# Kernel tuning notes

Hardware: AMD Instinct MI355X
Metric: run time of the kernel (lower is better)

## Reference

```python
import jax, jax.numpy as jnp
import numpy as np

EPS = 1e-6
T = 8            # max_recursion_depth
STACK = 16       # stack_size
K = 1024         # n_symbols
CC = 0.25        # commitment_cost
ETH_W = 0.005    # ethical_weight
PONDER = 1e-4    # ponder_penalty
B, DIM, V = 1024, 512, 32000


def _clin(Wr, Wi, zr, zi):
    # complex linear: (Wr + i Wi)(zr + i zi), nn.Linear convention x @ W.T
    return zr @ Wr.T - zi @ Wi.T, zi @ Wr.T + zr @ Wi.T


def _cnorm(scale, shift, zr, zi):
    mag = jnp.sqrt(zr * zr + zi * zi) + EPS
    mean = mag.mean(-1, keepdims=True)
    var = mag.var(-1, keepdims=True, ddof=1)  # torch.var unbiased=True
    nm = (mag - mean) / jnp.sqrt(var + EPS) * scale + shift
    ph = jnp.arctan2(zi, zr)
    return nm * jnp.cos(ph), nm * jnp.sin(ph)


def _modrelu(b, zr, zi):
    n = jnp.sqrt(zr * zr + zi * zi) + EPS
    s = jax.nn.relu(n + b) / n
    return zr * s, zi * s


def setup_inputs() -> dict:
    key = jax.random.key(0)
    ks = jax.random.split(key, 24)
    g = lambda k, sh, s=0.02: (jax.random.normal(k, sh, jnp.float32) * s)
    xav = lambda k, sh: jax.random.uniform(k, sh, jnp.float32, -1, 1) * np.sqrt(6.0 / (sh[0] + sh[1]))
    return {
        'input_ids': jax.random.randint(ks[0], (B, 1), 0, V),
        'emb_mag': g(ks[1], (V, DIM), 1.0),
        'emb_phase': g(ks[2], (V, DIM), 1.0),
        'lin_r': xav(ks[3], (DIM, DIM)), 'lin_i': xav(ks[4], (DIM, DIM)),
        'norm_scale': jnp.ones((DIM,), jnp.float32), 'norm_shift': jnp.zeros((DIM,), jnp.float32),
        'mod_bias': jnp.zeros((DIM,), jnp.float32),
        'halt_W': g(ks[5], (1, 2 * DIM)), 'halt_b': jnp.full((1,), -2.0, jnp.float32),
        'ctrl_W': g(ks[6], (3, 2 * DIM)), 'ctrl_b': jnp.zeros((3,), jnp.float32),
        'q_r': xav(ks[7], (DIM, DIM)), 'q_i': xav(ks[8], (DIM, DIM)),
        'k_r': xav(ks[9], (DIM, DIM)), 'k_i': xav(ks[10], (DIM, DIM)),
        'v_r': xav(ks[11], (DIM, DIM)), 'v_i': xav(ks[12], (DIM, DIM)),
        'codebook': jax.random.normal(ks[13], (K, 2 * DIM), jnp.float32),
        'adjacency': jnp.zeros((K, K), jnp.float32),
        'dec_W': g(ks[14], (V, 2 * DIM)), 'dec_b': jnp.zeros((V,), jnp.float32),
    }


def reference(input_ids, emb_mag, emb_phase, lin_r, lin_i, norm_scale, norm_shift, mod_bias,
              halt_W, halt_b, ctrl_W, ctrl_b, q_r, q_i, k_r, k_i, v_r, v_i,
              codebook, adjacency, dec_W, dec_b):
    dim = emb_mag.shape[1]
    b = input_ids.shape[0]
    idx = input_ids[:, 0]
    r, th = emb_mag[idx], emb_phase[idx]
    zr, zi = r * jnp.cos(th), r * jnp.sin(th)  # [B, dim] complex embedding

    mem = jnp.zeros((b, STACK, 2 * dim), zr.dtype)
    ptr = jnp.zeros((b, STACK), zr.dtype).at[:, 0].set(1.0)
    remain = jnp.ones((b, 1), zr.dtype)
    zwr = jnp.zeros_like(zr); zwi = jnp.zeros_like(zi)
    ponder = jnp.float32(0.0); vq_tot = jnp.float32(0.0)
    eth_tot = jnp.float32(0.0); prev = None
    scale = dim ** -0.5

    for step in range(T):
        # AdaptiveRecursiveCell: linear -> norm -> modrelu -> attention
        pr, pi = _clin(lin_r, lin_i, zr, zi)
        pr, pi = _cnorm(norm_scale, norm_shift, pr, pi)
        pr, pi = _modrelu(mod_bias, pr, pi)
        qr, qi = _clin(q_r, q_i, pr, pi)
        kr, ki = _clin(k_r, k_i, pr, pi)
        vr, vi = _clin(v_r, v_i, pr, pi)
        qf = jnp.concatenate([qr, qi], -1)
        kf = jnp.concatenate([kr, ki], -1)
        A = jax.nn.softmax(qf @ kf.T * scale, -1)  # [B, B] cross-batch attention
        pr, pi = A @ vr, A @ vi
        zf = jnp.concatenate([pr, pi], -1)  # [B, 2dim]
        halt = jax.nn.sigmoid(zf @ halt_W.T + halt_b)        # [B, 1]
        ctrl = jax.nn.softmax(zf @ ctrl_W.T + ctrl_b, -1)    # [B, 3]

        # DifferentiableStack
        push, pop, noop = ctrl[:, :1], ctrl[:, 1:2], ctrl[:, 2:3]
        ptr_up = jnp.roll(ptr, 1, axis=1)
        ptr_dn = jnp.roll(ptr, -1, axis=1)
        nptr = push * ptr_up + pop * ptr_dn + noop * ptr
        nptr = nptr / (nptr.sum(1, keepdims=True) + EPS)
        wm = push * ptr_up  # [B, STACK]
        mem = wm[:, :, None] * zf[:, None, :] + mem * (1.0 - wm[:, :, None])
        read = (mem * nptr[:, :, None]).sum(1)  # [B, 2dim]
        ptr = nptr
        cr = pr + read[:, :dim]; ci = pi + read[:, dim:]

        # GraphMemoryVQ (batched path: graph bias branch is a no-op)
        cf = jnp.concatenate([cr, ci], -1)
        d = ((cf * cf).sum(-1, keepdims=True) + (codebook * codebook).sum(-1)
             - 2.0 * cf @ codebook.T)  # [B, K]
        sym = jnp.argmin(d, -1)
        zq = codebook[sym]
        vq_tot = vq_tot + jnp.mean((zq - jax.lax.stop_gradient(cf)) ** 2) \
                 + CC * jnp.mean((jax.lax.stop_gradient(zq) - cf) ** 2)
        zq = cf + jax.lax.stop_gradient(zq - cf)  # straight-through
        sr, si = zq[:, :dim], zq[:, dim:]

        # EthicalConstraint: cross_entropy(adjacency[prev], curr)
        if prev is not None:
            row = adjacency[prev]  # [B, K]
            eth = jnp.mean(jax.nn.logsumexp(row, -1)
                           - jnp.take_along_axis(row, sym[:, None], 1)[:, 0])
            eth_tot = eth_tot + eth
        prev = sym

        # ACT weighting
        w = remain if step == T - 1 else halt * remain
        zwr = zwr + w * sr; zwi = zwi + w * si
        remain = remain * (1.0 - halt)
        ponder = ponder + remain.mean()
        zr, zi = sr, si

    logits = jnp.concatenate([zwr, zwi], -1) @ dec_W.T + dec_b  # [B, V]
    aux_loss = vq_tot + ETH_W * eth_tot + PONDER * ponder
    return logits, aux_loss
```

## Files before the change

kernel.cpp:

```cpp
#include <hip/hip_runtime.h>
#include <math.h>

#define NB 1024
#define ND 512
#define ND2 1024
#define NSTEPS 8
#define NSTACK 16
#define NK 1024
#define NV 32000
#define FEPS 1e-6f
#define ATT_SCALE 0.044194173824159216f

typedef _Float16 f16;
typedef f16 f16x8 __attribute__((ext_vector_type(8)));
typedef f16 f16x4 __attribute__((ext_vector_type(4)));
typedef float f32x4 __attribute__((ext_vector_type(4)));
typedef unsigned long long u64;

__device__ __forceinline__ int swz(int row, int chunk) {
    return row * 32 + ((chunk ^ ((row >> 1) & 3)) * 8);
}

__device__ __forceinline__ void gl16(const f16* g, f16* l) {
    __builtin_amdgcn_global_load_lds(
        (const __attribute__((address_space(1))) void*)g,
        (__attribute__((address_space(3))) void*)l, 16, 0, 0);
}

__device__ __forceinline__ u64 fkey(float v, int idx) {
    unsigned int ub = __float_as_uint(v);
    unsigned int ord = (ub & 0x80000000u) ? ~ub : (ub | 0x80000000u);
    return ((u64)ord << 32) | (unsigned int)idx;
}

__device__ __forceinline__ void amin_lds(u64* a, u64 k) {
    u64 old = *a;
    while (k < old) {
        u64 prev = atomicCAS(a, old, k);
        if (prev == old) break;
        old = prev;
    }
}

__device__ __forceinline__ float blk_sum(float v, float* red) {
    int t = threadIdx.x;
    red[t] = v; __syncthreads();
    for (int s = 128; s > 0; s >>= 1) {
        if (t < s) red[t] += red[t + s];
        __syncthreads();
    }
    float r = red[0]; __syncthreads();
    return r;
}

__device__ __forceinline__ float blk_max(float v, float* red) {
    int t = threadIdx.x;
    red[t] = v; __syncthreads();
    for (int s = 128; s > 0; s >>= 1) {
        if (t < s) red[t] = fmaxf(red[t], red[t + s]);
        __syncthreads();
    }
    float r = red[0]; __syncthreads();
    return r;
}

__device__ __forceinline__ void split_write(float v, f16* oh, f16* ol, size_t idx) {
    f16 h = (f16)v;
    oh[idx] = h;
    ol[idx] = (f16)((v - (float)h) * 1024.f);
}

__device__ __forceinline__ void buildW_elem(const float* Wr, const float* Wi,
                                            f16* oh, f16* ol, int transp, int idx) {
    int n = idx >> 10, k = idx & 1023;
    int r = transp ? k : n, c = transp ? n : k;
    float v;
    if (r < 512) v = (c < 512) ? Wr[r * 512 + c] : -Wi[r * 512 + (c - 512)];
    else { int r2 = r - 512; v = (c < 512) ? Wi[r2 * 512 + c] : Wr[r2 * 512 + (c - 512)]; }
    split_write(v, oh, ol, idx);
}

__global__ __launch_bounds__(256)
void k_setup(const int* __restrict__ ids, const float* __restrict__ mag,
             const float* __restrict__ phs,
             const float* __restrict__ lin_r, const float* __restrict__ lin_i,
             const float* __restrict__ q_r, const float* __restrict__ q_i,
             const float* __restrict__ k_r, const float* __restrict__ k_i,
             const float* __restrict__ v_r, const float* __restrict__ v_i,
             const float* __restrict__ cb, const float* __restrict__ adj,
             const float* __restrict__ dec_W,
             f16* __restrict__ W1_h, f16* __restrict__ W1_l,
             f16* __restrict__ WqT_h, f16* __restrict__ WqT_l,
             f16* __restrict__ WkT_h, f16* __restrict__ WkT_l,
             f16* __restrict__ Bv_h, f16* __restrict__ Bv_l,
             f16* __restrict__ cb_h, f16* __restrict__ cb_l,
             f16* __restrict__ dW_h,
             f16* __restrict__ zh, f16* __restrict__ zl,
             float* __restrict__ cbn, float* __restrict__ lse,
             float* __restrict__ ptrb, float* __restrict__ remainb,
             float* __restrict__ scal, u64* __restrict__ amin2) {
    __shared__ float red[256];
    int bid = blockIdx.x, t = threadIdx.x;
    if (bid < 4096) {
        buildW_elem(lin_r, lin_i, W1_h, W1_l, 0, bid * 256 + t);
    } else if (bid < 8192) {
        buildW_elem(q_r, q_i, WqT_h, WqT_l, 1, (bid - 4096) * 256 + t);
    } else if (bid < 12288) {
        buildW_elem(k_r, k_i, WkT_h, WkT_l, 1, (bid - 8192) * 256 + t);
    } else if (bid < 16384) {
        buildW_elem(v_r, v_i, Bv_h, Bv_l, 0, (bid - 12288) * 256 + t);
    } else if (bid < 20480) {
        int idx = (bid - 16384) * 256 + t;
        split_write(cb[idx], cb_h, cb_l, idx);
    } else if (bid < 22528) {
        size_t i = (size_t)(bid - 20480) * 256 + t;
        size_t st = (size_t)2048 * 256;
        size_t n = (size_t)NV * ND2;
        for (; i < n; i += st) dW_h[i] = (f16)dec_W[i];
    } else if (bid < 23552) {
        int k = bid - 22528;
        float s = 0.f;
        for (int c = t; c < ND2; c += 256) {
            float v = cb[(size_t)k * ND2 + c];
            s += v * v;
        }
        float tot = blk_sum(s, red);
        if (t == 0) cbn[k] = tot;
    } else if (bid < 24576) {
        int k = bid - 23552;
        float lm = -INFINITY;
        for (int c = t; c < NK; c += 256) lm = fmaxf(lm, adj[(size_t)k * NK + c]);
        float mxa = blk_max(lm, red);
        float le = 0.f;
        for (int c = t; c < NK; c += 256) le += expf(adj[(size_t)k * NK + c] - mxa);
        float se = blk_sum(le, red);
        if (t == 0) lse[k] = mxa + logf(se);
    } else if (bid < 25600) {
        int b = bid - 24576;
        int id = ids[b];
        for (int d = t; d < ND; d += 256) {
            float m = mag[(size_t)id * ND + d];
            float p = phs[(size_t)id * ND + d];
            split_write(m * cosf(p), zh, zl, (size_t)b * ND2 + d);
            split_write(m * sinf(p), zh, zl, (size_t)b * ND2 + ND + d);
        }
    } else {
        int i = (bid - 25600) * 256 + t;
        if (i < NB) {
            remainb[i] = 1.f;
            amin2[i] = ~0ULL;
            amin2[NB + i] = ~0ULL;
            for (int s = 0; s < NSTACK; ++s) ptrb[i * NSTACK + s] = (s == 0) ? 1.f : 0.f;
        }
        if (i < 8) scal[i] = 0.f;
    }
}

__global__ __launch_bounds__(256)
void k_split1(const float* __restrict__ in, f16* __restrict__ oh, f16* __restrict__ ol) {
    int idx = blockIdx.x * 256 + threadIdx.x;
    split_write(in[idx], oh, ol, idx);
}

template<int EPI>
__global__ __launch_bounds__(512, 4)
void k_sgemm5(const f16* __restrict__ Ah, const f16* __restrict__ Al,
              const f16* __restrict__ Bh, const f16* __restrict__ Bl,
              float* __restrict__ Cf,
              f16* __restrict__ qh, f16* __restrict__ ql,
              f16* __restrict__ vTh, f16* __restrict__ vTl,
              int N, int K, float alpha,
              const float* __restrict__ cbnv, u64* __restrict__ amin) {
    __shared__ f16 lds[2][2][4][64 * 32];
    __shared__ u64 aml[64];
    const int tid = threadIdx.x;
    const int g = tid >> 8;
    const int gt = tid & 255;
    const int srow = gt >> 2, scb = gt & 3;
    const int soff = swz(srow, scb);
    const int lane = tid & 63;
    const int q = (tid >> 6) & 3;
    const int qr = (q >> 1) * 32, qc = (q & 1) * 32;
    const int fr = lane & 15, cbk = lane >> 4;
    const int m0 = blockIdx.y * 64, n0 = blockIdx.x * 64;
    const int kbase = g * (K >> 1);
    const int iters = K >> 6;

    const f16* pA  = Ah + (size_t)(m0 + srow) * K + kbase + scb * 8;
    const f16* pAl_ = Al + (size_t)(m0 + srow) * K + kbase + scb * 8;
    const f16* pB  = Bh + (size_t)(n0 + srow) * K + kbase + scb * 8;
    const f16* pBl_ = Bl + (size_t)(n0 + srow) * K + kbase + scb * 8;

    f32x4 z4 = {0.f, 0.f, 0.f, 0.f};
    f32x4 acc0[2][2] = {{z4, z4}, {z4, z4}};
    f32x4 acc1[2][2] = {{z4, z4}, {z4, z4}};

    f16x8 rA  = *(const f16x8*)pA;
    f16x8 rAl = *(const f16x8*)pAl_;
    f16x8 rB  = *(const f16x8*)pB;
    f16x8 rBl = *(const f16x8*)pBl_;
    *(f16x8*)&lds[0][g][0][soff] = rA;
    *(f16x8*)&lds[0][g][1][soff] = rAl;
    *(f16x8*)&lds[0][g][2][soff] = rB;
    *(f16x8*)&lds[0][g][3][soff] = rBl;
    if (iters > 1) {
        rA  = *(const f16x8*)(pA + 32);
        rAl = *(const f16x8*)(pAl_ + 32);
        rB  = *(const f16x8*)(pB + 32);
        rBl = *(const f16x8*)(pBl_ + 32);
    }
    __syncthreads();

    for (int it = 0; it < iters; ++it) {
        const int cur = it & 1;
        f16x8 ah[2], al[2], bh[2], bl[2];
        #pragma unroll
        for (int i = 0; i < 2; ++i) {
            int ra = qr + i * 16 + fr;
            int oa = swz(ra, cbk);
            ah[i] = *(const f16x8*)&lds[cur][g][0][oa];
            al[i] = *(const f16x8*)&lds[cur][g][1][oa];
            int rb = qc + i * 16 + fr;
            int ob = swz(rb, cbk);
            bh[i] = *(const f16x8*)&lds[cur][g][2][ob];
            bl[i] = *(const f16x8*)&lds[cur][g][3][ob];
        }
        if (it + 1 < iters) {
            *(f16x8*)&lds[cur ^ 1][g][0][soff] = rA;
            *(f16x8*)&lds[cur ^ 1][g][1][soff] = rAl;
            *(f16x8*)&lds[cur ^ 1][g][2][soff] = rB;
            *(f16x8*)&lds[cur ^ 1][g][3][soff] = rBl;
            if (it + 2 < iters) {
                int ko = (it + 2) * 32;
                rA  = *(const f16x8*)(pA + ko);
                rAl = *(const f16x8*)(pAl_ + ko);
                rB  = *(const f16x8*)(pB + ko);
                rBl = *(const f16x8*)(pBl_ + ko);
            }
        }
        #pragma unroll
        for (int i = 0; i < 2; ++i)
            #pragma unroll
            for (int j = 0; j < 2; ++j) {
                acc0[i][j] = __builtin_amdgcn_mfma_f32_16x16x32_f16(ah[i], bh[j], acc0[i][j], 0, 0, 0);
                acc1[i][j] = __builtin_amdgcn_mfma_f32_16x16x32_f16(ah[i], bl[j], acc1[i][j], 0, 0, 0);
                acc1[i][j] = __builtin_amdgcn_mfma_f32_16x16x32_f16(al[i], bh[j], acc1[i][j], 0, 0, 0);
            }
        __syncthreads();
    }

    float val[2][2][4];
    #pragma unroll
    for (int i = 0; i < 2; ++i)
        #pragma unroll
        for (int j = 0; j < 2; ++j)
            #pragma unroll
            for (int jj = 0; jj < 4; ++jj)
                val[i][j][jj] = acc0[i][j][jj] + acc1[i][j][jj] * 9.765625e-4f;

    float* red = (float*)&lds[0][0][0][0];
    if (g == 1) {
        #pragma unroll
        for (int i = 0; i < 2; ++i)
            #pragma unroll
            for (int j = 0; j < 2; ++j) {
                int r = i * 16 + (lane >> 4) * 4, c = j * 16 + (lane & 15);
                #pragma unroll
                for (int jj = 0; jj < 4; ++jj)
                    red[q * 1056 + (r + jj) * 33 + c] = val[i][j][jj];
            }
        if constexpr (EPI == 3) {
            if (gt < 64) aml[gt] = ~0ULL;
        }
    }
    __syncthreads();
    if (g == 0) {
        #pragma unroll
        for (int i = 0; i < 2; ++i)
            #pragma unroll
            for (int j = 0; j < 2; ++j) {
                int r = i * 16 + (lane >> 4) * 4, c = j * 16 + (lane & 15);
                #pragma unroll
                for (int jj = 0; jj < 4; ++jj)
                    val[i][j][jj] += red[q * 1056 + (r + jj) * 33 + c];
                int orow = m0 + qr + r;
                int ocol = n0 + qc + c;
                if constexpr (EPI == 0) {
                    #pragma unroll
                    for (int jj = 0; jj < 4; ++jj)
                        Cf[(size_t)(orow + jj) * N + ocol] = alpha * val[i][j][jj];
                } else if constexpr (EPI == 2) {
                    int sec = ocol >> 10, lc = ocol & 1023;
                    if (sec == 0) {
                        #pragma unroll
                        for (int jj = 0; jj < 4; ++jj)
                            split_write(val[i][j][jj], qh, ql, (size_t)(orow + jj) * ND2 + lc);
                    } else {
                        f16x4 th, tl;
                        #pragma unroll
                        for (int jj = 0; jj < 4; ++jj) {
                            float v = val[i][j][jj];
                            f16 h = (f16)v;
                            th[jj] = h;
                            tl[jj] = (f16)((v - (float)h) * 1024.f);
                        }
                        *(f16x4*)&vTh[(size_t)lc * ND2 + orow] = th;
                        *(f16x4*)&vTl[(size_t)lc * ND2 + orow] = tl;
                    }
                } else {
                    float cbv = cbnv[ocol];
                    #pragma unroll
                    for (int jj = 0; jj < 4; ++jj) {
                        float v = cbv - 2.f * val[i][j][jj];
                        amin_lds(&aml[qr + r + jj], fkey(v, ocol));
                    }
                }
            }
    }
    if constexpr (EPI == 3) {
        __syncthreads();
        if (tid < 64) atomicMin(&amin[m0 + tid], aml[tid]);
    }
}

__global__ __launch_bounds__(512, 2)
void k_dgemm7(const f16* __restrict__ A, const f16* __restrict__ B,
              float* __restrict__ C, const float* __restrict__ bias) {
    __shared__ f16 sA[3][256 * 32];
    __shared__ f16 sB[3][128 * 32];
    const int bid = blockIdx.x;
    const int l2 = (bid & 7) * 125 + (bid >> 3);
    const int m0 = (l2 & 3) * 256;
    const int n0 = (l2 >> 2) * 128;
    const int tid = threadIdx.x;
    const int lane = tid & 63, w = tid >> 6;
    const int wr = (w >> 1) * 64, wc = (w & 1) * 64;
    const int fr = lane & 15, cbk = lane >> 4;
    const int K = ND2;
    const int srow = lane >> 2, pch = lane & 3;

    f32x4 z4 = {0.f, 0.f, 0.f, 0.f};
    f32x4 acc[4][4];
    #pragma unroll
    for (int i = 0; i < 4; ++i)
        #pragma unroll
        for (int j = 0; j < 4; ++j) acc[i][j] = z4;

    auto STAGE = [&](int itn, int nbuf) {
        int ko = itn * 32;
        #pragma unroll
        for (int c = 0; c < 3; ++c) {
            int m = w * 3 + c;
            if (m < 16) {
                int row = m * 16 + srow;
                int chunk = (pch ^ ((row >> 1) & 3)) * 8;
                gl16(A + (size_t)(m0 + row) * K + ko + chunk, (f16*)&sA[nbuf][m * 512]);
            } else {
                int mm = m - 16;
                int row = mm * 16 + srow;
                int chunk = (pch ^ ((row >> 1) & 3)) * 8;
                gl16(B + (size_t)(n0 + row) * K + ko + chunk, (f16*)&sB[nbuf][mm * 512]);
            }
        }
    };

    auto COMPUTE = [&](int buf) {
        f16x8 a[4], b[4];
        #pragma unroll
        for (int i = 0; i < 4; ++i) {
            int rra = wr + i * 16 + fr;
            a[i] = *(const f16x8*)&sA[buf][swz(rra, cbk)];
        }
        #pragma unroll
        for (int j = 0; j < 4; ++j) {
            int rrb = wc + j * 16 + fr;
            b[j] = *(const f16x8*)&sB[buf][swz(rrb, cbk)];
        }
        #pragma unroll
        for (int i = 0; i < 4; ++i)
            #pragma unroll
            for (int j = 0; j < 4; ++j)
                acc[i][j] = __builtin_amdgcn_mfma_f32_16x16x32_f16(a[i], b[j], acc[i][j], 0, 0, 0);
    };

    STAGE(0, 0);
    STAGE(1, 1);
    asm volatile("s_waitcnt vmcnt(3)" ::: "memory");
    __builtin_amdgcn_sched_barrier(0);
    __builtin_amdgcn_s_barrier();

    for (int it = 0; it < 30; ++it) {
        const int cur = it % 3;
        STAGE(it + 2, (it + 2) % 3);
        COMPUTE(cur);
        asm volatile("s_waitcnt vmcnt(3)" ::: "memory");
        __builtin_amdgcn_sched_barrier(0);
        __builtin_amdgcn_s_barrier();
    }
    COMPUTE(0);
    asm volatile("s_waitcnt vmcnt(0)" ::: "memory");
    __builtin_amdgcn_sched_barrier(0);
    __builtin_amdgcn_s_barrier();
    COMPUTE(1);

    #pragma unroll
    for (int i = 0; i < 4; ++i)
        #pragma unroll
        for (int j = 0; j < 4; ++j) {
            int orow = m0 + wr + i * 16 + (lane >> 4) * 4;
            int ocol = n0 + wc + j * 16 + (lane & 15);
            float bv = bias[ocol];
            #pragma unroll
            for (int jj = 0; jj < 4; ++jj)
                C[(size_t)(orow + jj) * NV + ocol] = acc[i][j][jj] + bv;
        }
}

__global__ __launch_bounds__(256)
void k_cnorm(const float* __restrict__ p, const float* __restrict__ CW1,
             const int* __restrict__ sym,
             f16* __restrict__ ph, f16* __restrict__ pl,
             const float* __restrict__ scale, const float* __restrict__ shift,
             const float* __restrict__ mbias) {
    __shared__ float red[256];
    int b = blockIdx.x, t = threadIdx.x;
    const float* row = sym ? (CW1 + (size_t)sym[b] * ND2) : (p + (size_t)b * ND2);
    float xr[2], xi[2], hv[2];
    float lsum = 0.f;
    #pragma unroll
    for (int l = 0; l < 2; ++l) {
        int d = t + l * 256;
        float a = row[d], c = row[ND + d];
        xr[l] = a; xi[l] = c;
        float h = sqrtf(a * a + c * c);
        hv[l] = h;
        lsum += h + FEPS;
    }
    float mean = blk_sum(lsum, red) * (1.f / ND);
    float lvar = 0.f;
    #pragma unroll
    for (int l = 0; l < 2; ++l) {
        float dv = (hv[l] + FEPS) - mean;
        lvar += dv * dv;
    }
    float var = blk_sum(lvar, red) * (1.f / (ND - 1));
    float istd = 1.f / sqrtf(var + FEPS);
    #pragma unroll
    for (int l = 0; l < 2; ++l) {
        int d = t + l * 256;
        float nm = ((hv[l] + FEPS) - mean) * istd * scale[d] + shift[d];
        float cc, ss;
        if (hv[l] > 0.f) { cc = xr[l] / hv[l]; ss = xi[l] / hv[l]; }
        else             { cc = 1.f; ss = 0.f; }
        float vr_ = nm * cc, vi_ = nm * ss;
        float n = sqrtf(vr_ * vr_ + vi_ * vi_) + FEPS;
        float aarg = n + mbias[d];
        float sg = (aarg > 0.f ? aarg : 0.f) / n;
        split_write(vr_ * sg, ph, pl, (size_t)b * ND2 + d);
        split_write(vi_ * sg, ph, pl, (size_t)b * ND2 + ND + d);
    }
}

__global__ __launch_bounds__(256)
void k_softmax(const float* __restrict__ S, f16* __restrict__ Ah, f16* __restrict__ Al) {
    __shared__ float red[256];
    int row = blockIdx.x, t = threadIdx.x;
    float v[4];
    float lm = -INFINITY;
    #pragma unroll
    for (int l = 0; l < 4; ++l) {
        v[l] = S[(size_t)row * NB + t + l * 256];
        lm = fmaxf(lm, v[l]);
    }
    float mx = blk_max(lm, red);
    float ls = 0.f;
    #pragma unroll
    for (int l = 0; l < 4; ++l) { v[l] = expf(v[l] - mx); ls += v[l]; }
    float tot = blk_sum(ls, red);
    float inv = 1024.f / tot;
    #pragma unroll
    for (int l = 0; l < 4; ++l)
        split_write(v[l] * inv, Ah, Al, (size_t)row * NB + t + l * 256);
}

__global__ __launch_bounds__(256)
void k_stack2(const float* __restrict__ zfh, int step,
              const float* __restrict__ hW, const float* __restrict__ hB,
              const float* __restrict__ cW, const float* __restrict__ cB,
              float* __restrict__ ptrb, float* __restrict__ Ptab,
              float* __restrict__ haltb, float* __restrict__ cfn,
              f16* __restrict__ cfh, f16* __restrict__ cfl) {
    __shared__ float zfs[ND2];
    __shared__ float red[256];
    __shared__ float pt[NSTACK], npv[NSTACK], wmv[NSTACK];
    __shared__ float coef[NSTEPS];
    __shared__ float snorm;
    int b = blockIdx.x, t = threadIdx.x;
    const float* zf = zfh + (size_t)step * NB * ND2 + (size_t)b * ND2;
    for (int c = t; c < ND2; c += 256) zfs[c] = zf[c];
    __syncthreads();
    float dh = 0, d0 = 0, d1 = 0, d2 = 0;
    for (int c = t; c < ND2; c += 256) {
        float z = zfs[c];
        dh += z * hW[c];
        d0 += z * cW[c];
        d1 += z * cW[ND2 + c];
        d2 += z * cW[2 * ND2 + c];
    }
    dh = blk_sum(dh, red);
    d0 = blk_sum(d0, red);
    d1 = blk_sum(d1, red);
    d2 = blk_sum(d2, red);
    float h = 1.f / (1.f + expf(-(dh + hB[0])));
    float l0 = d0 + cB[0], l1 = d1 + cB[1], l2 = d2 + cB[2];
    float mx = fmaxf(l0, fmaxf(l1, l2));
    float e0 = expf(l0 - mx), e1 = expf(l1 - mx), e2 = expf(l2 - mx);
    float es = e0 + e1 + e2;
    float push = e0 / es, pop = e1 / es, noop = e2 / es;
    if (t < NSTACK) pt[t] = ptrb[b * NSTACK + t];
    __syncthreads();
    if (t < NSTACK) {
        float up = pt[(t + NSTACK - 1) & 15];
        float dn = pt[(t + 1) & 15];
        npv[t] = push * up + pop * dn + noop * pt[t];
        wmv[t] = push * up;
    }
    __syncthreads();
    if (t == 0) {
        float s = 0.f;
        for (int j = 0; j < NSTACK; ++j) s += npv[j];
        snorm = 1.f / (s + FEPS);
    }
    __syncthreads();
    if (t < NSTACK) {
        npv[t] *= snorm;
        ptrb[b * NSTACK + t] = npv[t];
        float om = 1.f - wmv[t];
        for (int u = 0; u < step; ++u)
            Ptab[((size_t)b * NSTEPS + u) * NSTACK + t] *= om;
        Ptab[((size_t)b * NSTEPS + step) * NSTACK + t] = wmv[t];
    }
    __syncthreads();
    if (t <= step) {
        float s = 0.f;
        #pragma unroll
        for (int j = 0; j < NSTACK; ++j)
            s += npv[j] * Ptab[((size_t)b * NSTEPS + t) * NSTACK + j];
        coef[t] = s;
    }
    __syncthreads();
    float lq = 0.f;
    for (int c = t; c < ND2; c += 256) {
        float rd = coef[step] * zfs[c];
        for (int u = 0; u < step; ++u)
            rd += coef[u] * zfh[(size_t)u * NB * ND2 + (size_t)b * ND2 + c];
        float v = zfs[c] + rd;
        split_write(v, cfh, cfl, (size_t)b * ND2 + c);
        lq += v * v;
    }
    float q = blk_sum(lq, red);
    if (t == 0) { cfn[b] = q; haltb[b] = h; }
}

__global__ __launch_bounds__(256)
void k_vqatt(const u64* __restrict__ aminCur, u64* __restrict__ aminNxt,
             const float* __restrict__ SS,
             const f16* __restrict__ VTh, const f16* __restrict__ VTl,
             f16* __restrict__ Ah, f16* __restrict__ Al,
             f16* __restrict__ vTh, f16* __restrict__ vTl,
             const float* __restrict__ cb, const float* __restrict__ cfn,
             const float* __restrict__ adj, const float* __restrict__ lse,
             const float* __restrict__ haltb,
             float* __restrict__ remainb, float* __restrict__ zw,
             f16* __restrict__ zwh, f16* __restrict__ zwl,
             int* __restrict__ prev, float* __restrict__ scal,
             int step, int islast) {
    __shared__ float red[256];
    __shared__ int syms[NB];
    int t = threadIdx.x;
    if (blockIdx.x < NB) {
        int b = blockIdx.x;
        u64 key = aminCur[b];
        int sym = (int)(key & 0xFFFFFFFFu);
        unsigned int ord = (unsigned int)(key >> 32);
        unsigned int ub = (ord & 0x80000000u) ? (ord & 0x7FFFFFFFu) : ~ord;
        float sval0 = __uint_as_float(ub);
        float sdt = sval0 + cfn[b];
        float contrib = 0.f;
        if (step > 0) {
            int pv = prev[b];
            contrib = lse[pv] - adj[(size_t)pv * NK + sym];
        }
        float hb = haltb[b];
        float rm = remainb[b];
        float w = islast ? rm : hb * rm;
        for (int c = t; c < ND2; c += 256) {
            size_t idx = (size_t)b * ND2 + c;
            float nv = zw[idx] + w * cb[(size_t)sym * ND2 + c];
            if (islast) split_write(nv, zwh, zwl, idx);
            else zw[idx] = nv;
        }
        if (t == 0) {
            float nrm = rm * (1.f - hb);
            remainb[b] = nrm;
            atomicAdd(&scal[0], sdt);
            if (step > 0) atomicAdd(&scal[1], contrib);
            atomicAdd(&scal[2], nrm);
            prev[b] = sym;
            aminNxt[b] = ~0ULL;
        }
    } else {
        for (int i = t; i < NB; i += 256) syms[i] = (int)(aminCur[i] & 0xFFFFFFFFu);
        __syncthreads();
        if (blockIdx.x < 2 * NB) {
            int row = blockIdx.x - NB;
            const float* Srow = SS + (size_t)syms[row] * NK;
            float v[4];
            float lm = -INFINITY;
            #pragma unroll
            for (int l = 0; l < 4; ++l) {
                v[l] = ATT_SCALE * Srow[syms[t + l * 256]];
                lm = fmaxf(lm, v[l]);
            }
            float mx = blk_max(lm, red);
            float ls = 0.f;
            #pragma unroll
            for (int l = 0; l < 4; ++l) { v[l] = expf(v[l] - mx); ls += v[l]; }
            float tot = blk_sum(ls, red);
            float inv = 1024.f / tot;
            #pragma unroll
            for (int l = 0; l < 4; ++l)
                split_write(v[l] * inv, Ah, Al, (size_t)row * NB + t + l * 256);
        } else {
            int n = blockIdx.x - 2 * NB;
            const f16* rh = VTh + (size_t)n * NK;
            const f16* rl = VTl + (size_t)n * NK;
            for (int b = t; b < NB; b += 256) {
                int s = syms[b];
                vTh[(size_t)n * NB + b] = rh[s];
                vTl[(size_t)n * NB + b] = rl[s];
            }
        }
    }
}

__global__ void k_aux(const float* __restrict__ scal, float* __restrict__ out) {
    out[0] = 1.25f * scal[0] / (1024.f * 1024.f)
           + 0.005f * (scal[1] / 1024.f)
           + 0.0001f * (scal[2] / 1024.f);
}

extern "C" void kernel_launch(void* const* d_in, const int* in_sizes, int n_in,
                              void* d_out, int out_size, void* d_ws, size_t ws_size,
                              hipStream_t stream) {
    const int*   input_ids  = (const int*)  d_in[0];
    const float* emb_mag    = (const float*)d_in[1];
    const float* emb_phase  = (const float*)d_in[2];
    const float* lin_r      = (const float*)d_in[3];
    const float* lin_i      = (const float*)d_in[4];
    const float* norm_scale = (const float*)d_in[5];
    const float* norm_shift = (const float*)d_in[6];
    const float* mod_bias   = (const float*)d_in[7];
    const float* halt_W     = (const float*)d_in[8];
    const float* halt_b     = (const float*)d_in[9];
    const float* ctrl_W     = (const float*)d_in[10];
    const float* ctrl_b     = (const float*)d_in[11];
    const float* q_r        = (const float*)d_in[12];
    const float* q_i        = (const float*)d_in[13];
    const float* k_r        = (const float*)d_in[14];
    const float* k_i        = (const float*)d_in[15];
    const float* v_r        = (const float*)d_in[16];
    const float* v_i        = (const float*)d_in[17];
    const float* codebook   = (const float*)d_in[18];
    const float* adjacency  = (const float*)d_in[19];
    const float* dec_W      = (const float*)d_in[20];
    const float* dec_b      = (const float*)d_in[21];
    float* out = (float*)d_out;

    float* fb = (float*)d_ws;
    size_t o = 0;
    auto af = [&](size_t n) { float* p = fb + o; o += n; return p; };
    float* scr      = af((size_t)NB * ND2);
    float* SS       = af((size_t)NK * NK);
    float* zfh      = af((size_t)NSTEPS * NB * ND2);
    float* CW1      = af((size_t)NK * ND2);
    float* zw       = af((size_t)NB * ND2);
    float* Ptab     = af((size_t)NB * NSTEPS * NSTACK);
    float* ptrb     = af((size_t)NB * NSTACK);
    float* haltb    = af(NB);
    float* remainb  = af(NB);
    float* cbn      = af(NK);
    float* cfn      = af(NB);
    float* lse      = af(NK);
    int*   prev     = (int*)af(NB);
    u64*   amin2    = (u64*)af(4 * NB);
    float* scal     = af(8);

    f16* hbuf = (f16*)(fb + o);
    size_t ho = 0;
    auto ah = [&](size_t n) { f16* q = hbuf + ho; ho += n; return q; };
    f16* z_h   = ah((size_t)NB * ND2);
    f16* z_l   = ah((size_t)NB * ND2);
    f16* p_h   = ah((size_t)NB * ND2);
    f16* p_l   = ah((size_t)NB * ND2);
    f16* t_h   = ah((size_t)NB * ND2);
    f16* t_l   = ah((size_t)NB * ND2);
    f16* vT_h  = ah((size_t)NB * ND2);
    f16* vT_l  = ah((size_t)NB * ND2);
    f16* VTt_h = ah((size_t)ND2 * NK);
    f16* VTt_l = ah((size_t)ND2 * NK);
    f16* Pn_h  = ah((size_t)NK * ND2);
    f16* Pn_l  = ah((size_t)NK * ND2);
    f16* A_h   = ah((size_t)NB * NB);
    f16* A_l   = ah((size_t)NB * NB);
    f16* cf_h  = ah((size_t)NB * ND2);
    f16* cf_l  = ah((size_t)NB * ND2);
    f16* zw_h  = ah((size_t)NB * ND2);
    f16* zw_l  = ah((size_t)NB * ND2);
    f16* W1_h  = ah((size_t)ND2 * ND2);
    f16* W1_l  = ah((size_t)ND2 * ND2);
    f16* WqT_h = ah((size_t)ND2 * ND2);
    f16* WqT_l = ah((size_t)ND2 * ND2);
    f16* WkT_h = ah((size_t)ND2 * ND2);
    f16* WkT_l = ah((size_t)ND2 * ND2);
    f16* Bc_h  = ah((size_t)2 * ND2 * ND2);
    f16* Bc_l  = ah((size_t)2 * ND2 * ND2);
    f16* cb_h  = ah((size_t)NK * ND2);
    f16* cb_l  = ah((size_t)NK * ND2);
    f16* dW_h  = ah((size_t)NV * ND2);

    hipMemsetAsync(zw, 0, (size_t)NB * ND2 * sizeof(float), stream);
    k_setup<<<25604, 256, 0, stream>>>(input_ids, emb_mag, emb_phase,
        lin_r, lin_i, q_r, q_i, k_r, k_i, v_r, v_i, codebook, adjacency, dec_W,
        W1_h, W1_l, WqT_h, WqT_l, WkT_h, WkT_l,
        Bc_h + (size_t)ND2 * ND2, Bc_l + (size_t)ND2 * ND2,
        cb_h, cb_l, dW_h, z_h, z_l, cbn, lse, ptrb, remainb, scal, amin2);
    k_sgemm5<0><<<dim3(16, 16), 512, 0, stream>>>(WkT_h, WkT_l, WqT_h, WqT_l, scr,
        nullptr, nullptr, nullptr, nullptr, ND2, ND2, 1.f, nullptr, nullptr);
    k_split1<<<(ND2 * ND2) / 256, 256, 0, stream>>>(scr, Bc_h, Bc_l);
    k_sgemm5<0><<<dim3(16, 16), 512, 0, stream>>>(cb_h, cb_l, W1_h, W1_l, CW1,
        nullptr, nullptr, nullptr, nullptr, ND2, ND2, 1.f, nullptr, nullptr);
    k_cnorm<<<NK, 256, 0, stream>>>(CW1, nullptr, nullptr, Pn_h, Pn_l,
                                    norm_scale, norm_shift, mod_bias);
    k_sgemm5<2><<<dim3(32, 16), 512, 0, stream>>>(Pn_h, Pn_l, Bc_h, Bc_l, nullptr,
        t_h, t_l, VTt_h, VTt_l, 2 * ND2, ND2, 1.f, nullptr, nullptr);
    k_sgemm5<0><<<dim3(16, 16), 512, 0, stream>>>(t_h, t_l, Pn_h, Pn_l, SS,
        nullptr, nullptr, nullptr, nullptr, NK, ND2, 1.f, nullptr, nullptr);

    for (int step = 0; step < NSTEPS; ++step) {
        if (step == 0) {
            k_sgemm5<0><<<dim3(16, 16), 512, 0, stream>>>(z_h, z_l, W1_h, W1_l, scr,
                nullptr, nullptr, nullptr, nullptr, ND2, ND2, 1.f, nullptr, nullptr);
            k_cnorm<<<NB, 256, 0, stream>>>(scr, nullptr, nullptr, p_h, p_l,
                                            norm_scale, norm_shift, mod_bias);
            k_sgemm5<2><<<dim3(32, 16), 512, 0, stream>>>(p_h, p_l, Bc_h, Bc_l, nullptr,
                t_h, t_l, vT_h, vT_l, 2 * ND2, ND2, 1.f, nullptr, nullptr);
            k_sgemm5<0><<<dim3(16, 16), 512, 0, stream>>>(t_h, t_l, p_h, p_l, scr,
                nullptr, nullptr, nullptr, nullptr, NB, ND2, ATT_SCALE, nullptr, nullptr);
            k_softmax<<<NB, 256, 0, stream>>>(scr, A_h, A_l);
        }
        k_sgemm5<0><<<dim3(16, 16), 512, 0, stream>>>(A_h, A_l, vT_h, vT_l,
            zfh + (size_t)step * NB * ND2,
            nullptr, nullptr, nullptr, nullptr, ND2, NB, 9.765625e-4f, nullptr, nullptr);
        k_stack2<<<NB, 256, 0, stream>>>(zfh, step, halt_W, halt_b, ctrl_W, ctrl_b,
                                         ptrb, Ptab, haltb, cfn, cf_h, cf_l);
        k_sgemm5<3><<<dim3(16, 16), 512, 0, stream>>>(cf_h, cf_l, cb_h, cb_l, nullptr,
            nullptr, nullptr, nullptr, nullptr, NK, ND2, 1.f, cbn,
            amin2 + (size_t)(step & 1) * NB);
        int islast = (step == NSTEPS - 1) ? 1 : 0;
        int grid = islast ? NB : 3 * NB;
        k_vqatt<<<grid, 256, 0, stream>>>(amin2 + (size_t)(step & 1) * NB,
                                          amin2 + (size_t)((step + 1) & 1) * NB,
                                          SS, VTt_h, VTt_l, A_h, A_l, vT_h, vT_l,
                                          codebook, cfn, adjacency, lse, haltb, remainb,
                                          zw, zw_h, zw_l, prev, scal, step, islast);
    }
    k_dgemm7<<<1000, 512, 0, stream>>>(zw_h, dW_h, out, dec_b);
    k_aux<<<1, 1, 0, stream>>>(scal, out + (size_t)NB * NV);
}
```

Baseline: 1.154 ms.

## Triple-buffer split-fp16 GEMM with direct global-to-LDS async loads

Replaces the register-staged double-buffered K loop in the split-precision GEMM with a three-stage LDS ring filled by global_load_lds. Each wave loads one of the four operand planes, and manual vmcnt waits plus barriers keep two stages in flight ahead of compute. This aims to hide global latency and free the registers used for staging. In exchange it uses more LDS, drops occupancy hints from 4 to 2 blocks, and hardcodes 16 iterations, which assumes K=1024 for every call.

```diff
diff --git a/kernel.cpp b/kernel.cpp
--- a/kernel.cpp
+++ b/kernel.cpp
@@ -163,80 +163,56 @@
 }
 
 template<int EPI>
-__global__ __launch_bounds__(512, 4)
-void k_sgemm5(const f16* __restrict__ Ah, const f16* __restrict__ Al,
+__global__ __launch_bounds__(512, 2)
+void k_sgemm9(const f16* __restrict__ Ah, const f16* __restrict__ Al,
               const f16* __restrict__ Bh, const f16* __restrict__ Bl,
               float* __restrict__ Cf,
               f16* __restrict__ qh, f16* __restrict__ ql,
               f16* __restrict__ vTh, f16* __restrict__ vTl,
               int N, int K, float alpha,
               const float* __restrict__ cbnv, u64* __restrict__ amin) {
-    __shared__ f16 lds[2][2][4][64 * 32];
+    __shared__ f16 lds[3][2][4][64 * 32];
     __shared__ u64 aml[64];
     const int tid = threadIdx.x;
     const int g = tid >> 8;
-    const int gt = tid & 255;
-    const int srow = gt >> 2, scb = gt & 3;
-    const int soff = swz(srow, scb);
     const int lane = tid & 63;
     const int q = (tid >> 6) & 3;
     const int qr = (q >> 1) * 32, qc = (q & 1) * 32;
     const int fr = lane & 15, cbk = lane >> 4;
     const int m0 = blockIdx.y * 64, n0 = blockIdx.x * 64;
     const int kbase = g * (K >> 1);
-    const int iters = K >> 6;
-
-    const f16* pA  = Ah + (size_t)(m0 + srow) * K + kbase + scb * 8;
-    const f16* pAl_ = Al + (size_t)(m0 + srow) * K + kbase + scb * 8;
-    const f16* pB  = Bh + (size_t)(n0 + srow) * K + kbase + scb * 8;
-    const f16* pBl_ = Bl + (size_t)(n0 + srow) * K + kbase + scb * 8;
+
+    const f16* sbase = (q == 0) ? Ah : (q == 1) ? Al : (q == 2) ? Bh : Bl;
+    const int rbase = (q < 2) ? m0 : n0;
+    const int srow = lane >> 2, pch = lane & 3;
 
     f32x4 z4 = {0.f, 0.f, 0.f, 0.f};
     f32x4 acc0[2][2] = {{z4, z4}, {z4, z4}};
     f32x4 acc1[2][2] = {{z4, z4}, {z4, z4}};
 
-    f16x8 rA  = *(const f16x8*)pA;
-    f16x8 rAl = *(const f16x8*)pAl_;
-    f16x8 rB  = *(const f16x8*)pB;
-    f16x8 rBl = *(const f16x8*)pBl_;
-    *(f16x8*)&lds[0][g][0][soff] = rA;
-    *(f16x8*)&lds[0][g][1][soff] = rAl;
-    *(f16x8*)&lds[0][g][2][soff] = rB;
-    *(f16x8*)&lds[0][g][3][soff] = rBl;
-    if (iters > 1) {
-        rA  = *(const f16x8*)(pA + 32);
-        rAl = *(const f16x8*)(pAl_ + 32);
-        rB  = *(const f16x8*)(pB + 32);
-        rBl = *(const f16x8*)(pBl_ + 32);
-    }
-    __syncthreads();
-
-    for (int it = 0; it < iters; ++it) {
-        const int cur = it & 1;
+    auto STAGE = [&](int itn, int nbuf) {
+        int ko = kbase + itn * 32;
+        #pragma unroll
+        for (int c = 0; c < 4; ++c) {
+            int row = c * 16 + srow;
+            int chunk = (pch ^ ((row >> 1) & 3)) * 8;
+            gl16(sbase + (size_t)(rbase + row) * K + ko + chunk,
+                 (f16*)&lds[nbuf][g][q][c * 512]);
+        }
+    };
+
+    auto COMPUTE = [&](int buf) {
         f16x8 ah[2], al[2], bh[2], bl[2];
         #pragma unroll
         for (int i = 0; i < 2; ++i) {
             int ra = qr + i * 16 + fr;
             int oa = swz(ra, cbk);
-            ah[i] = *(const f16x8*)&lds[cur][g][0][oa];
-            al[i] = *(const f16x8*)&lds[cur][g][1][oa];
+            ah[i] = *(const f16x8*)&lds[buf][g][0][oa];
+            al[i] = *(const f16x8*)&lds[buf][g][1][oa];
             int rb = qc + i * 16 + fr;
             int ob = swz(rb, cbk);
-            bh[i] = *(const f16x8*)&lds[cur][g][2][ob];
-            bl[i] = *(const f16x8*)&lds[cur][g][3][ob];
-        }
-        if (it + 1 < iters) {
-            *(f16x8*)&lds[cur ^ 1][g][0][soff] = rA;
-            *(f16x8*)&lds[cur ^ 1][g][1][soff] = rAl;
-            *(f16x8*)&lds[cur ^ 1][g][2][soff] = rB;
-            *(f16x8*)&lds[cur ^ 1][g][3][soff] = rBl;
-            if (it + 2 < iters) {
-                int ko = (it + 2) * 32;
-                rA  = *(const f16x8*)(pA + ko);
-                rAl = *(const f16x8*)(pAl_ + ko);
-                rB  = *(const f16x8*)(pB + ko);
-                rBl = *(const f16x8*)(pBl_ + ko);
-            }
+            bh[i] = *(const f16x8*)&lds[buf][g][2][ob];
+            bl[i] = *(const f16x8*)&lds[buf][g][3][ob];
         }
         #pragma unroll
         for (int i = 0; i < 2; ++i)
@@ -246,8 +222,27 @@
                 acc1[i][j] = __builtin_amdgcn_mfma_f32_16x16x32_f16(ah[i], bl[j], acc1[i][j], 0, 0, 0);
                 acc1[i][j] = __builtin_amdgcn_mfma_f32_16x16x32_f16(al[i], bh[j], acc1[i][j], 0, 0, 0);
             }
-        __syncthreads();
-    }
+    };
+
+    STAGE(0, 0);
+    STAGE(1, 1);
+    asm volatile("s_waitcnt vmcnt(4)" ::: "memory");
+    __builtin_amdgcn_sched_barrier(0);
+    __builtin_amdgcn_s_barrier();
+
+    for (int it = 0; it < 14; ++it) {
+        STAGE(it + 2, (it + 2) % 3);
+        COMPUTE(it % 3);
+        asm volatile("s_waitcnt vmcnt(4)" ::: "memory");
+        __builtin_amdgcn_sched_barrier(0);
+        __builtin_amdgcn_s_barrier();
+    }
+    COMPUTE(14 % 3);
+    asm volatile("s_waitcnt vmcnt(0)" ::: "memory");
+    __builtin_amdgcn_sched_barrier(0);
+    __builtin_amdgcn_s_barrier();
+    COMPUTE(15 % 3);
+    __syncthreads();
 
     float val[2][2][4];
     #pragma unroll
@@ -270,7 +265,7 @@
                     red[q * 1056 + (r + jj) * 33 + c] = val[i][j][jj];
             }
         if constexpr (EPI == 3) {
-            if (gt < 64) aml[gt] = ~0ULL;
+            if ((tid & 255) < 64) aml[tid & 255] = ~0ULL;
         }
     }
     __syncthreads();
@@ -735,36 +730,36 @@
         W1_h, W1_l, WqT_h, WqT_l, WkT_h, WkT_l,
         Bc_h + (size_t)ND2 * ND2, Bc_l + (size_t)ND2 * ND2,
         cb_h, cb_l, dW_h, z_h, z_l, cbn, lse, ptrb, remainb, scal, amin2);
-    k_sgemm5<0><<<dim3(16, 16), 512, 0, stream>>>(WkT_h, WkT_l, WqT_h, WqT_l, scr,
+    k_sgemm9<0><<<dim3(16, 16), 512, 0, stream>>>(WkT_h, WkT_l, WqT_h, WqT_l, scr,
         nullptr, nullptr, nullptr, nullptr, ND2, ND2, 1.f, nullptr, nullptr);
     k_split1<<<(ND2 * ND2) / 256, 256, 0, stream>>>(scr, Bc_h, Bc_l);
-    k_sgemm5<0><<<dim3(16, 16), 512, 0, stream>>>(cb_h, cb_l, W1_h, W1_l, CW1,
+    k_sgemm9<0><<<dim3(16, 16), 512, 0, stream>>>(cb_h, cb_l, W1_h, W1_l, CW1,
         nullptr, nullptr, nullptr, nullptr, ND2, ND2, 1.f, nullptr, nullptr);
     k_cnorm<<<NK, 256, 0, stream>>>(CW1, nullptr, nullptr, Pn_h, Pn_l,
                                     norm_scale, norm_shift, mod_bias);
-    k_sgemm5<2><<<dim3(32, 16), 512, 0, stream>>>(Pn_h, Pn_l, Bc_h, Bc_l, nullptr,
+    k_sgemm9<2><<<dim3(32, 16), 512, 0, stream>>>(Pn_h, Pn_l, Bc_h, Bc_l, nullptr,
         t_h, t_l, VTt_h, VTt_l, 2 * ND2, ND2, 1.f, nullptr, nullptr);
-    k_sgemm5<0><<<dim3(16, 16), 512, 0, stream>>>(t_h, t_l, Pn_h, Pn_l, SS,
+    k_sgemm9<0><<<dim3(16, 16), 512, 0, stream>>>(t_h, t_l, Pn_h, Pn_l, SS,
         nullptr, nullptr, nullptr, nullptr, NK, ND2, 1.f, nullptr, nullptr);
 
     for (int step = 0; step < NSTEPS; ++step) {
         if (step == 0) {
-            k_sgemm5<0><<<dim3(16, 16), 512, 0, stream>>>(z_h, z_l, W1_h, W1_l, scr,
+            k_sgemm9<0><<<dim3(16, 16), 512, 0, stream>>>(z_h, z_l, W1_h, W1_l, scr,
                 nullptr, nullptr, nullptr, nullptr, ND2, ND2, 1.f, nullptr, nullptr);
             k_cnorm<<<NB, 256, 0, stream>>>(scr, nullptr, nullptr, p_h, p_l,
                                             norm_scale, norm_shift, mod_bias);
-            k_sgemm5<2><<<dim3(32, 16), 512, 0, stream>>>(p_h, p_l, Bc_h, Bc_l, nullptr,
+            k_sgemm9<2><<<dim3(32, 16), 512, 0, stream>>>(p_h, p_l, Bc_h, Bc_l, nullptr,
                 t_h, t_l, vT_h, vT_l, 2 * ND2, ND2, 1.f, nullptr, nullptr);
-            k_sgemm5<0><<<dim3(16, 16), 512, 0, stream>>>(t_h, t_l, p_h, p_l, scr,
+            k_sgemm9<0><<<dim3(16, 16), 512, 0, stream>>>(t_h, t_l, p_h, p_l, scr,
                 nullptr, nullptr, nullptr, nullptr, NB, ND2, ATT_SCALE, nullptr, nullptr);
             k_softmax<<<NB, 256, 0, stream>>>(scr, A_h, A_l);
         }
-        k_sgemm5<0><<<dim3(16, 16), 512, 0, stream>>>(A_h, A_l, vT_h, vT_l,
+        k_sgemm9<0><<<dim3(16, 16), 512, 0, stream>>>(A_h, A_l, vT_h, vT_l,
             zfh + (size_t)step * NB * ND2,
             nullptr, nullptr, nullptr, nullptr, ND2, NB, 9.765625e-4f, nullptr, nullptr);
         k_stack2<<<NB, 256, 0, stream>>>(zfh, step, halt_W, halt_b, ctrl_W, ctrl_b,
                                          ptrb, Ptab, haltb, cfn, cf_h, cf_l);
-        k_sgemm5<3><<<dim3(16, 16), 512, 0, stream>>>(cf_h, cf_l, cb_h, cb_l, nullptr,
+        k_sgemm9<3><<<dim3(16, 16), 512, 0, stream>>>(cf_h, cf_l, cb_h, cb_l, nullptr,
             nullptr, nullptr, nullptr, nullptr, NK, ND2, 1.f, cbn,
             amin2 + (size_t)(step & 1) * NB);
         int islast = (step == NSTEPS - 1) ? 1 : 0;
```

After: 1.151 ms. About the same (-0.3%).
